# Kernel tuning notes

Hardware: AMD Instinct MI355X
Metric: run time of the kernel (lower is better)

## Reference

```python
import jax, jax.numpy as jnp
import numpy as np

I, H1, H2, O = 64, 1024, 1024, 64

def lstm_cell(x, h, c, W_ih, W_hh, b_ih, b_hh):
    # PyTorch LSTMCell: gates ordered i, f, g, o
    gates = x @ W_ih.T + b_ih + h @ W_hh.T + b_hh  # [B, 4H]
    i, f, g, o = jnp.split(gates, 4, axis=-1)
    i = jax.nn.sigmoid(i)
    f = jax.nn.sigmoid(f)
    g = jnp.tanh(g)
    o = jax.nn.sigmoid(o)
    c_new = f * c + i * g
    h_new = o * jnp.tanh(c_new)
    return h_new, c_new

def setup_inputs() -> dict:
    key = jax.random.key(0)
    ks = jax.random.split(key, 11)
    s1 = 1.0 / np.sqrt(H1)
    s2 = 1.0 / np.sqrt(H2)
    u = lambda k, shape, s: jax.random.uniform(k, shape, jnp.float32, -s, s)
    return {
        "inputs": jax.random.normal(ks[0], (128, 512, I), jnp.float32),
        "W_ih1": u(ks[1], (4 * H1, I), s1),
        "W_hh1": u(ks[2], (4 * H1, H1), s1),
        "b_ih1": u(ks[3], (4 * H1,), s1),
        "b_hh1": u(ks[4], (4 * H1,), s1),
        "W_ih2": u(ks[5], (4 * H2, H1), s2),
        "W_hh2": u(ks[6], (4 * H2, H2), s2),
        "b_ih2": u(ks[7], (4 * H2,), s2),
        "b_hh2": u(ks[8], (4 * H2,), s2),
        "W_out": u(ks[9], (O, H2), s2),
        "b_out": u(ks[10], (O,), s2),
    }

def reference(inputs, W_ih1, W_hh1, b_ih1, b_hh1, W_ih2, W_hh2, b_ih2, b_hh2, W_out, b_out):
    B = inputs.shape[0]
    h1 = jnp.zeros((B, H1), inputs.dtype)
    c1 = jnp.zeros((B, H1), inputs.dtype)
    h2 = jnp.zeros((B, H2), inputs.dtype)
    c2 = jnp.zeros((B, H2), inputs.dtype)

    def step(carry, x_t):
        h1, c1, h2, c2 = carry
        h1, c1 = lstm_cell(x_t, h1, c1, W_ih1, W_hh1, b_ih1, b_hh1)
        h2, c2 = lstm_cell(h1, h2, c2, W_ih2, W_hh2, b_ih2, b_hh2)
        y = h2 @ W_out.T + b_out  # [B, O]
        return (h1, c1, h2, c2), y

    xs = jnp.swapaxes(inputs, 0, 1)  # [T, B, I]
    _, ys = jax.lax.scan(step, (h1, c1, h2, c2), xs)
    return jnp.swapaxes(ys, 0, 1)  # [B, T, O]
```

## Files before the change

### kernel.cpp

```cpp
#include <hip/hip_runtime.h>
#include <hip/hip_fp16.h>

typedef _Float16 half8 __attribute__((ext_vector_type(8)));
typedef float    float4_ __attribute__((ext_vector_type(4)));

#define TSTEPS 512
#define NA 64
#define NB 128
#define NC 8
#define FSTRIDE 32

#define FLA_OFF   0
#define FLB_OFF   8192
#define FLC_OFF   24576
#define H1_OFF    32768
#define H1_PHASE  262144
#define H2_OFF    (H1_OFF + 2 * H1_PHASE)
#define X_OFF     (H2_OFF + 2 * H1_PHASE)
#define X_TSTRIDE 16384
#define ZERO_BYTES X_OFF

__device__ __forceinline__ float fastrcp(float x) {
    float r; asm("v_rcp_f32 %0, %1" : "=v"(r) : "v"(x)); return r;
}
__device__ __forceinline__ float sigf(float x)  { return fastrcp(1.0f + __expf(-x)); }
__device__ __forceinline__ float tanh_(float x) { return 1.0f - 2.0f * fastrcp(1.0f + __expf(2.0f * x)); }

__device__ __forceinline__ half8 wfrag_load(const float* Wa, int lda,
                                            const float* Wb, int ldb,
                                            int split, int row, int k0) {
    const float* s = (k0 < split) ? (Wa + (size_t)row * lda + k0)
                                  : (Wb + (size_t)row * ldb + (k0 - split));
    float4_ lo = *(const float4_*)s;
    float4_ hi = *(const float4_*)(s + 4);
    half8 r;
    r[0] = (_Float16)lo[0]; r[1] = (_Float16)lo[1];
    r[2] = (_Float16)lo[2]; r[3] = (_Float16)lo[3];
    r[4] = (_Float16)hi[0]; r[5] = (_Float16)hi[1];
    r[6] = (_Float16)hi[2]; r[7] = (_Float16)hi[3];
    return r;
}


__device__ __forceinline__ half8 ldg_sc1_16(const void* p) {
    half8 r;
    asm volatile("global_load_dwordx4 %0, %1, off sc1" : "=v"(r) : "v"(p));
    return r;
}

#define VMWAIT8(A) asm volatile("s_waitcnt vmcnt(0)" : \
    "+v"((A)[0]), "+v"((A)[1]), "+v"((A)[2]), "+v"((A)[3]), \
    "+v"((A)[4]), "+v"((A)[5]), "+v"((A)[6]), "+v"((A)[7]) :: "memory")

#define VMWAIT2_N(G, NS) asm volatile("s_waitcnt vmcnt(" NS ")" : \
    "+v"((G)[0]), "+v"((G)[1]) :: "memory")

__device__ __forceinline__ void stg_coh_16(void* p, float4_ v) {
    asm volatile("global_store_dwordx4 %0, %1, off sc0 sc1" :: "v"(p), "v"(v) : "memory");
}

__device__ __forceinline__ void stg_coh_int(void* p, int v) {
    asm volatile("global_store_dword %0, %1, off sc0 sc1" :: "v"(p), "v"(v) : "memory");
}

__device__ __forceinline__ void publish(int* fbase, int idx, int v) {
    asm volatile("s_waitcnt vmcnt(0)" ::: "memory");
    __syncthreads();
    if (threadIdx.x == 0) stg_coh_int(fbase + idx * FSTRIDE, v);
}

__device__ __forceinline__ int ld_flag(const int* f, int idx) {
    return __hip_atomic_load(f + idx * FSTRIDE, __ATOMIC_RELAXED,
                             __HIP_MEMORY_SCOPE_AGENT);
}

__device__ __forceinline__ void waitA(const int* fA, const int* fB, int t) {
    if (threadIdx.x < 64) {
        const int lane = threadIdx.x;
        for (;;) {
            int a  = ld_flag(fA, lane);
            int b0 = ld_flag(fB, lane);
            int b1 = ld_flag(fB, 64 + lane);
            if (__all((a >= t) && (b0 >= t - 1) && (b1 >= t - 1))) break;
            __builtin_amdgcn_s_sleep(1);
        }
    }
    __syncthreads();
}

__device__ __forceinline__ void waitB(const int* fA, const int* fB, const int* fC, int t) {
    if (threadIdx.x < 64) {
        const int lane = threadIdx.x;
        for (;;) {
            int a  = ld_flag(fA, lane);
            int b0 = ld_flag(fB, lane);
            int b1 = ld_flag(fB, 64 + lane);
            int c  = ld_flag(fC, lane & 7);
            if (__all((a >= t + 1) && (b0 >= t) && (b1 >= t) && (c >= t - 1))) break;
            __builtin_amdgcn_s_sleep(1);
        }
    }
    __syncthreads();
}

__device__ __forceinline__ void waitC(const int* fB, int t) {
    if (threadIdx.x < 64) {
        const int lane = threadIdx.x;
        for (;;) {
            int b0 = ld_flag(fB, lane);
            int b1 = ld_flag(fB, 64 + lane);
            if (__all((b0 >= t + 1) && (b1 >= t + 1))) break;
            __builtin_amdgcn_s_sleep(1);
        }
    }
    __syncthreads();
}

__device__ __forceinline__ int swz(int u) {
    return u ^ (((u >> 3) ^ (u >> 7)) & 7);
}

extern "C" __global__ void prep_x(const float* __restrict__ in, char* __restrict__ ws) {
    const int t = blockIdx.x;
    char* X = ws + X_OFF + (size_t)t * X_TSTRIDE;
    for (int idx = threadIdx.x; idx < 8192; idx += 256) {
        int kt = idx >> 12, rem = idx & 4095;
        int quad = rem >> 10, rem2 = rem & 1023;
        int b = rem2 >> 3, j = rem2 & 7;
        int i = kt * 32 + quad * 8 + j;
        float v = in[(size_t)b * 32768 + (size_t)t * 64 + i];
        *(_Float16*)(X + (size_t)idx * 2) = (_Float16)v;
    }
}

extern "C" __global__ __launch_bounds__(256, 1)
void lstm_persistent(const float* __restrict__ Wih1, const float* __restrict__ Whh1,
                     const float* __restrict__ bih1, const float* __restrict__ bhh1,
                     const float* __restrict__ Wih2, const float* __restrict__ Whh2,
                     const float* __restrict__ bih2, const float* __restrict__ bhh2,
                     const float* __restrict__ Wout, const float* __restrict__ bout,
                     char* __restrict__ ws, float* __restrict__ out) {
    const int tid = threadIdx.x;
    const int w = tid >> 6, lane = tid & 63;
    const int quad = lane >> 4, cl = lane & 15;
    const int laneoff = quad * 2048 + cl * 16;
    int* fA = (int*)(ws + FLA_OFF);
    int* fB = (int*)(ws + FLB_OFF);
    int* fC = (int*)(ws + FLC_OFF);
    char* H1 = ws + H1_OFF;
    char* H2 = ws + H2_OFF;
    char* X  = ws + X_OFF;
    const int blk = blockIdx.x;
    __shared__ __align__(16) char smem[143360];

    if (blk < NA) {
        char* wlds = smem;
        unsigned short* stga = (unsigned short*)(smem + 139264);
        const int c0 = blk * 16;
        for (int f = tid; f < 8704; f += 256) {
            int kk = f >> 8, rem = f & 255, nt = rem >> 6, ln = rem & 63;
            int row = nt * 1024 + c0 + (ln & 15);
            int k0 = kk * 32 + (ln >> 4) * 8;
            *(half8*)(wlds + (size_t)f * 16) = wfrag_load(Wih1, 64, Whh1, 1024, 64, row, k0);
        }
        __syncthreads();
        float ba[4];
#pragma unroll
        for (int g = 0; g < 4; ++g) ba[g] = bih1[g * 1024 + c0 + cl] + bhh1[g * 1024 + c0 + cl];
        float cst[2][4];
#pragma unroll
        for (int mi = 0; mi < 2; ++mi)
#pragma unroll
            for (int r = 0; r < 4; ++r) cst[mi][r] = 0.0f;
        const int mtb0 = (2 * w) * 256, mtb1 = (2 * w + 1) * 256;

        for (int t = 0; t < TSTEPS; ++t) {
            waitA(fA, fB, t);

            const char* xb  = X + (size_t)t * X_TSTRIDE;
            const char* h1r = H1 + (((t & 1) ^ 1) ? H1_PHASE : 0);
            char*       h1w = H1 + ((t & 1) ? H1_PHASE : 0);

            half8 af[10][2];
#pragma unroll
            for (int p = 0; p < 10; ++p) {
                const char* bp = (p < 2) ? (xb + p * 8192) : (h1r + (p - 2) * 8192);
                af[p][0] = ldg_sc1_16(bp + laneoff + mtb0);
                af[p][1] = ldg_sc1_16(bp + laneoff + mtb1);
            }
            float4_ acc[2][4];
#pragma unroll
            for (int mi = 0; mi < 2; ++mi)
#pragma unroll
                for (int nt = 0; nt < 4; ++nt) acc[mi][nt] = (float4_){0.f, 0.f, 0.f, 0.f};
#pragma unroll
            for (int kk = 0; kk < 34; ++kk) {
                const int cur = kk % 10;
                if (kk <= 24)      { VMWAIT2_N(af[cur], "18"); }
                else if (kk == 25) { VMWAIT2_N(af[cur], "16"); }
                else if (kk == 26) { VMWAIT2_N(af[cur], "14"); }
                else if (kk == 27) { VMWAIT2_N(af[cur], "12"); }
                else if (kk == 28) { VMWAIT2_N(af[cur], "10"); }
                else if (kk == 29) { VMWAIT2_N(af[cur], "8");  }
                else if (kk == 30) { VMWAIT2_N(af[cur], "6");  }
                else if (kk == 31) { VMWAIT2_N(af[cur], "4");  }
                else if (kk == 32) { VMWAIT2_N(af[cur], "2");  }
                else               { VMWAIT2_N(af[cur], "0");  }
                half8 wl0 = *(const half8*)(wlds + (size_t)((kk * 4 + 0) * 64 + lane) * 16);
                half8 wl1 = *(const half8*)(wlds + (size_t)((kk * 4 + 1) * 64 + lane) * 16);
                half8 wl2 = *(const half8*)(wlds + (size_t)((kk * 4 + 2) * 64 + lane) * 16);
                half8 wl3 = *(const half8*)(wlds + (size_t)((kk * 4 + 3) * 64 + lane) * 16);
                acc[0][0] = __builtin_amdgcn_mfma_f32_16x16x32_f16(af[cur][0], wl0, acc[0][0], 0, 0, 0);
                acc[0][1] = __builtin_amdgcn_mfma_f32_16x16x32_f16(af[cur][0], wl1, acc[0][1], 0, 0, 0);
                acc[0][2] = __builtin_amdgcn_mfma_f32_16x16x32_f16(af[cur][0], wl2, acc[0][2], 0, 0, 0);
                acc[0][3] = __builtin_amdgcn_mfma_f32_16x16x32_f16(af[cur][0], wl3, acc[0][3], 0, 0, 0);
                acc[1][0] = __builtin_amdgcn_mfma_f32_16x16x32_f16(af[cur][1], wl0, acc[1][0], 0, 0, 0);
                acc[1][1] = __builtin_amdgcn_mfma_f32_16x16x32_f16(af[cur][1], wl1, acc[1][1], 0, 0, 0);
                acc[1][2] = __builtin_amdgcn_mfma_f32_16x16x32_f16(af[cur][1], wl2, acc[1][2], 0, 0, 0);
                acc[1][3] = __builtin_amdgcn_mfma_f32_16x16x32_f16(af[cur][1], wl3, acc[1][3], 0, 0, 0);
                if (kk + 10 < 34) {
                    const int kn = kk + 10;
                    const char* bn = (kn < 2) ? (xb + kn * 8192) : (h1r + (kn - 2) * 8192);
                    af[cur][0] = ldg_sc1_16(bn + laneoff + mtb0);
                    af[cur][1] = ldg_sc1_16(bn + laneoff + mtb1);
                }
            }
#pragma unroll
            for (int mi = 0; mi < 2; ++mi) {
#pragma unroll
                for (int r = 0; r < 4; ++r) {
                    float iv = acc[mi][0][r] + ba[0];
                    float fv = acc[mi][1][r] + ba[1];
                    float gv = acc[mi][2][r] + ba[2];
                    float ov = acc[mi][3][r] + ba[3];
                    float c = sigf(fv) * cst[mi][r] + sigf(iv) * tanh_(gv);
                    float h = sigf(ov) * tanh_(c);
                    cst[mi][r] = c;
                    int m = (2 * w + mi) * 16 + quad * 4 + r;
                    int u = ((cl >> 3) << 7) + m;
                    union { _Float16 hh; unsigned short us; } uu;
                    uu.hh = (_Float16)h;
                    stga[swz(u) * 8 + (cl & 7)] = uu.us;
                }
            }
            __syncthreads();
            {
                const int g = tid >> 7, b = tid & 127;
                int u = (g << 7) + b;
                float4_ v = *(const float4_*)(stga + swz(u) * 8);
                char* dst = h1w + ((c0 >> 5) << 13) + ((((c0 >> 3) + g) & 3) << 11) + (b << 4);
                stg_coh_16(dst, v);
            }
            publish(fA, blk, t + 1);
        }
    } else if (blk < NA + NB) {
        char* wldsB = smem;
        unsigned short* stgb = (unsigned short*)(smem + 131072);
        const int bb = blk - NA;
        const int c0 = bb * 8;
        for (int f = tid; f < 8192; f += 256) {
            int kk = f >> 7, rem = f & 127, pr = rem >> 6, ln = rem & 63;
            int cl_ = ln & 15;
            int colB_ = c0 + (cl_ & 7);
            int row = (pr == 0) ? ((cl_ < 8) ? colB_ : (1024 + colB_))
                                : ((cl_ < 8) ? (2048 + colB_) : (3072 + colB_));
            int k0 = kk * 32 + (ln >> 4) * 8;
            *(half8*)(wldsB + (size_t)f * 16) = wfrag_load(Wih2, 1024, Whh2, 1024, 1024, row, k0);
        }
        __syncthreads();
        const int colB = c0 + (cl & 7);
        const float bi = bih2[colB] + bhh2[colB];
        const float bf = bih2[1024 + colB] + bhh2[1024 + colB];
        const float bg = bih2[2048 + colB] + bhh2[2048 + colB];
        const float bo = bih2[3072 + colB] + bhh2[3072 + colB];
        float cst[2][4];
#pragma unroll
        for (int mi = 0; mi < 2; ++mi)
#pragma unroll
            for (int r = 0; r < 4; ++r) cst[mi][r] = 0.0f;
        const bool lolane = (cl & 8) == 0;
        const int mtb0 = (2 * w) * 256, mtb1 = (2 * w + 1) * 256;

        for (int t = 0; t < TSTEPS; ++t) {
            waitB(fA, fB, fC, t);

            const char* h1c = H1 + ((t & 1) ? H1_PHASE : 0);
            const char* h2r = H2 + (((t & 1) ^ 1) ? H1_PHASE : 0);
            char*       h2w = H2 + ((t & 1) ? H1_PHASE : 0);

            half8 af[12][2];
#pragma unroll
            for (int p = 0; p < 12; ++p) {
                const char* bp = h1c + p * 8192;
                af[p][0] = ldg_sc1_16(bp + laneoff + mtb0);
                af[p][1] = ldg_sc1_16(bp + laneoff + mtb1);
            }
            float4_ acc[2][2];
#pragma unroll
            for (int mi = 0; mi < 2; ++mi) {
                acc[mi][0] = (float4_){0.f, 0.f, 0.f, 0.f};
                acc[mi][1] = (float4_){0.f, 0.f, 0.f, 0.f};
            }
#pragma unroll
            for (int kk = 0; kk < 64; ++kk) {
                const int cur = kk % 12;
                if (kk <= 52)      { VMWAIT2_N(af[cur], "22"); }
                else if (kk == 53) { VMWAIT2_N(af[cur], "20"); }
                else if (kk == 54) { VMWAIT2_N(af[cur], "18"); }
                else if (kk == 55) { VMWAIT2_N(af[cur], "16"); }
                else if (kk == 56) { VMWAIT2_N(af[cur], "14"); }
                else if (kk == 57) { VMWAIT2_N(af[cur], "12"); }
                else if (kk == 58) { VMWAIT2_N(af[cur], "10"); }
                else if (kk == 59) { VMWAIT2_N(af[cur], "8");  }
                else if (kk == 60) { VMWAIT2_N(af[cur], "6");  }
                else if (kk == 61) { VMWAIT2_N(af[cur], "4");  }
                else if (kk == 62) { VMWAIT2_N(af[cur], "2");  }
                else               { VMWAIT2_N(af[cur], "0");  }
                half8 wl0 = *(const half8*)(wldsB + (size_t)((kk * 2 + 0) * 64 + lane) * 16);
                half8 wl1 = *(const half8*)(wldsB + (size_t)((kk * 2 + 1) * 64 + lane) * 16);
                acc[0][0] = __builtin_amdgcn_mfma_f32_16x16x32_f16(af[cur][0], wl0, acc[0][0], 0, 0, 0);
                acc[0][1] = __builtin_amdgcn_mfma_f32_16x16x32_f16(af[cur][0], wl1, acc[0][1], 0, 0, 0);
                acc[1][0] = __builtin_amdgcn_mfma_f32_16x16x32_f16(af[cur][1], wl0, acc[1][0], 0, 0, 0);
                acc[1][1] = __builtin_amdgcn_mfma_f32_16x16x32_f16(af[cur][1], wl1, acc[1][1], 0, 0, 0);
                if (kk + 12 < 64) {
                    const int kn = kk + 12;
                    const char* bn = (kn < 32) ? (h1c + kn * 8192) : (h2r + (kn - 32) * 8192);
                    af[cur][0] = ldg_sc1_16(bn + laneoff + mtb0);
                    af[cur][1] = ldg_sc1_16(bn + laneoff + mtb1);
                }
            }
#pragma unroll
            for (int mi = 0; mi < 2; ++mi) {
#pragma unroll
                for (int r = 0; r < 4; ++r) {
                    float d0 = acc[mi][0][r], d1 = acc[mi][1][r];
                    float s0 = __shfl_xor(d0, 8, 64);
                    float s1 = __shfl_xor(d1, 8, 64);
                    float iv = (lolane ? d0 : s0) + bi;
                    float fv = (lolane ? s0 : d0) + bf;
                    float gv = (lolane ? d1 : s1) + bg;
                    float ov = (lolane ? s1 : d1) + bo;
                    float c = sigf(fv) * cst[mi][r] + sigf(iv) * tanh_(gv);
                    float h = sigf(ov) * tanh_(c);
                    cst[mi][r] = c;
                    if (lolane) {
                        int m = (2 * w + mi) * 16 + quad * 4 + r;
                        union { _Float16 hh; unsigned short us; } uu;
                        uu.hh = (_Float16)h;
                        stgb[swz(m) * 8 + (cl & 7)] = uu.us;
                    }
                }
            }
            __syncthreads();
            if (tid < 128) {
                const int b = tid;
                float4_ v = *(const float4_*)(stgb + swz(b) * 8);
                char* dst = h2w + ((c0 >> 5) << 13) + (((c0 >> 3) & 3) << 11) + (b << 4);
                stg_coh_16(dst, v);
            }
            publish(fB, bb, t + 1);
        }
    } else {
        float* redc = (float*)smem;
        const int cb = blk - NA - NB;
        const int kbase = w * 8;
        half8 wfr[4][8];
#pragma unroll
        for (int nt = 0; nt < 4; ++nt) {
            int row = nt * 16 + cl;
#pragma unroll
            for (int kk = 0; kk < 8; ++kk)
                wfr[nt][kk] = wfrag_load(Wout, 1024, Wout, 1024, 1 << 30, row, (kbase + kk) * 32 + quad * 8);
        }
        const float bo_ = bout[w * 16 + cl];

        for (int t = 0; t < TSTEPS; ++t) {
            waitC(fB, t);
            const char* h2c = H2 + ((t & 1) ? H1_PHASE : 0);
            float4_ acc[4];
#pragma unroll
            for (int nt = 0; nt < 4; ++nt) acc[nt] = (float4_){0.f, 0.f, 0.f, 0.f};
            half8 af[8];
#pragma unroll
            for (int kk = 0; kk < 8; ++kk)
                af[kk] = ldg_sc1_16(h2c + (kbase + kk) * 8192 + laneoff + cb * 256);
            VMWAIT8(af);
#pragma unroll
            for (int kk = 0; kk < 8; ++kk)
#pragma unroll
                for (int nt = 0; nt < 4; ++nt)
                    acc[nt] = __builtin_amdgcn_mfma_f32_16x16x32_f16(af[kk], wfr[nt][kk], acc[nt], 0, 0, 0);
#pragma unroll
            for (int r = 0; r < 4; ++r) {
                if (w != r) *(float4_*)&redc[(w * 64 + lane) * 4] = acc[r];
                __syncthreads();
                if (w == r) {
#pragma unroll
                    for (int wo = 0; wo < 4; ++wo) if (wo != r)
                        acc[r] += *(const float4_*)&redc[(wo * 64 + lane) * 4];
                }
                __syncthreads();
            }
            float4_ myy = acc[0];
#pragma unroll
            for (int r = 1; r < 4; ++r) if (w == r) myy = acc[r];
#pragma unroll
            for (int r = 0; r < 4; ++r) {
                int m = cb * 16 + quad * 4 + r;
                out[(size_t)m * 32768 + (size_t)t * 64 + (w * 16 + cl)] = myy[r] + bo_;
            }
            publish(fC, cb, t + 1);
        }
    }
}

extern "C" void kernel_launch(void* const* d_in, const int* in_sizes, int n_in,
                              void* d_out, int out_size, void* d_ws, size_t ws_size,
                              hipStream_t stream) {
    const float* inp  = (const float*)d_in[0];
    const float* Wih1 = (const float*)d_in[1];
    const float* Whh1 = (const float*)d_in[2];
    const float* bih1 = (const float*)d_in[3];
    const float* bhh1 = (const float*)d_in[4];
    const float* Wih2 = (const float*)d_in[5];
    const float* Whh2 = (const float*)d_in[6];
    const float* bih2 = (const float*)d_in[7];
    const float* bhh2 = (const float*)d_in[8];
    const float* Wout = (const float*)d_in[9];
    const float* bout = (const float*)d_in[10];
    char* ws = (char*)d_ws;

    hipMemsetAsync(d_ws, 0, ZERO_BYTES, stream);
    prep_x<<<TSTEPS, 256, 0, stream>>>(inp, ws);
    lstm_persistent<<<NA + NB + NC, 256, 0, stream>>>(Wih1, Whh1, bih1, bhh1,
                                                      Wih2, Whh2, bih2, bhh2,
                                                      Wout, bout, ws, (float*)d_out);
}
```

Measured before the change: 4.270 ms.

## Split layer-2 wait so recurrent h2 matmul overlaps waiting on layer-1 output

Layer 2 used to wait for both its own recurrent dependencies and the fresh layer-1 h1 before starting any work. The wait is now split in two. It first waits only on the h2/flag dependencies and computes the W_hh2·h2 half of the gates. Only then does it wait for layer-1 h1 and compute the W_ih2·h1 half, which takes layer-1 latency off the critical path. Prefetch depth also grows (14 buffers in layer 1, 16 in layer 2), which raises register pressure and could reduce occupancy or cause spills.

```diff
diff --git a/kernel.cpp b/kernel.cpp
--- a/kernel.cpp
+++ b/kernel.cpp
@@ -88,15 +88,26 @@
     __syncthreads();
 }
 
-__device__ __forceinline__ void waitB(const int* fA, const int* fB, const int* fC, int t) {
+__device__ __forceinline__ void waitB1(const int* fB, const int* fC, int t) {
     if (threadIdx.x < 64) {
         const int lane = threadIdx.x;
         for (;;) {
-            int a  = ld_flag(fA, lane);
             int b0 = ld_flag(fB, lane);
             int b1 = ld_flag(fB, 64 + lane);
             int c  = ld_flag(fC, lane & 7);
-            if (__all((a >= t + 1) && (b0 >= t) && (b1 >= t) && (c >= t - 1))) break;
+            if (__all((b0 >= t) && (b1 >= t) && (c >= t - 1))) break;
+            __builtin_amdgcn_s_sleep(1);
+        }
+    }
+    __syncthreads();
+}
+
+__device__ __forceinline__ void waitB2(const int* fA, int t) {
+    if (threadIdx.x < 64) {
+        const int lane = threadIdx.x;
+        for (;;) {
+            int a = ld_flag(fA, lane);
+            if (__all(a >= t + 1)) break;
             __builtin_amdgcn_s_sleep(1);
         }
     }
@@ -181,9 +192,9 @@
             const char* h1r = H1 + (((t & 1) ^ 1) ? H1_PHASE : 0);
             char*       h1w = H1 + ((t & 1) ? H1_PHASE : 0);
 
-            half8 af[10][2];
-#pragma unroll
-            for (int p = 0; p < 10; ++p) {
+            half8 af[14][2];
+#pragma unroll
+            for (int p = 0; p < 14; ++p) {
                 const char* bp = (p < 2) ? (xb + p * 8192) : (h1r + (p - 2) * 8192);
                 af[p][0] = ldg_sc1_16(bp + laneoff + mtb0);
                 af[p][1] = ldg_sc1_16(bp + laneoff + mtb1);
@@ -195,8 +206,12 @@
                 for (int nt = 0; nt < 4; ++nt) acc[mi][nt] = (float4_){0.f, 0.f, 0.f, 0.f};
 #pragma unroll
             for (int kk = 0; kk < 34; ++kk) {
-                const int cur = kk % 10;
-                if (kk <= 24)      { VMWAIT2_N(af[cur], "18"); }
+                const int cur = kk % 14;
+                if (kk <= 20)      { VMWAIT2_N(af[cur], "26"); }
+                else if (kk == 21) { VMWAIT2_N(af[cur], "24"); }
+                else if (kk == 22) { VMWAIT2_N(af[cur], "22"); }
+                else if (kk == 23) { VMWAIT2_N(af[cur], "20"); }
+                else if (kk == 24) { VMWAIT2_N(af[cur], "18"); }
                 else if (kk == 25) { VMWAIT2_N(af[cur], "16"); }
                 else if (kk == 26) { VMWAIT2_N(af[cur], "14"); }
                 else if (kk == 27) { VMWAIT2_N(af[cur], "12"); }
@@ -218,9 +233,9 @@
                 acc[1][1] = __builtin_amdgcn_mfma_f32_16x16x32_f16(af[cur][1], wl1, acc[1][1], 0, 0, 0);
                 acc[1][2] = __builtin_amdgcn_mfma_f32_16x16x32_f16(af[cur][1], wl2, acc[1][2], 0, 0, 0);
                 acc[1][3] = __builtin_amdgcn_mfma_f32_16x16x32_f16(af[cur][1], wl3, acc[1][3], 0, 0, 0);
-                if (kk + 10 < 34) {
-                    const int kn = kk + 10;
-                    const char* bn = (kn < 2) ? (xb + kn * 8192) : (h1r + (kn - 2) * 8192);
+                if (kk + 14 < 34) {
+                    const int kn = kk + 14;
+                    const char* bn = h1r + (kn - 2) * 8192;
                     af[cur][0] = ldg_sc1_16(bn + laneoff + mtb0);
                     af[cur][1] = ldg_sc1_16(bn + laneoff + mtb1);
                 }
@@ -282,53 +297,98 @@
         const int mtb0 = (2 * w) * 256, mtb1 = (2 * w + 1) * 256;
 
         for (int t = 0; t < TSTEPS; ++t) {
-            waitB(fA, fB, fC, t);
-
             const char* h1c = H1 + ((t & 1) ? H1_PHASE : 0);
             const char* h2r = H2 + (((t & 1) ^ 1) ? H1_PHASE : 0);
             char*       h2w = H2 + ((t & 1) ? H1_PHASE : 0);
 
-            half8 af[12][2];
-#pragma unroll
-            for (int p = 0; p < 12; ++p) {
-                const char* bp = h1c + p * 8192;
-                af[p][0] = ldg_sc1_16(bp + laneoff + mtb0);
-                af[p][1] = ldg_sc1_16(bp + laneoff + mtb1);
-            }
             float4_ acc[2][2];
 #pragma unroll
             for (int mi = 0; mi < 2; ++mi) {
                 acc[mi][0] = (float4_){0.f, 0.f, 0.f, 0.f};
                 acc[mi][1] = (float4_){0.f, 0.f, 0.f, 0.f};
             }
-#pragma unroll
-            for (int kk = 0; kk < 64; ++kk) {
-                const int cur = kk % 12;
-                if (kk <= 52)      { VMWAIT2_N(af[cur], "22"); }
-                else if (kk == 53) { VMWAIT2_N(af[cur], "20"); }
-                else if (kk == 54) { VMWAIT2_N(af[cur], "18"); }
-                else if (kk == 55) { VMWAIT2_N(af[cur], "16"); }
-                else if (kk == 56) { VMWAIT2_N(af[cur], "14"); }
-                else if (kk == 57) { VMWAIT2_N(af[cur], "12"); }
-                else if (kk == 58) { VMWAIT2_N(af[cur], "10"); }
-                else if (kk == 59) { VMWAIT2_N(af[cur], "8");  }
-                else if (kk == 60) { VMWAIT2_N(af[cur], "6");  }
-                else if (kk == 61) { VMWAIT2_N(af[cur], "4");  }
-                else if (kk == 62) { VMWAIT2_N(af[cur], "2");  }
-                else               { VMWAIT2_N(af[cur], "0");  }
+            half8 af[16][2];
+
+            waitB1(fB, fC, t);
+#pragma unroll
+            for (int p = 0; p < 16; ++p) {
+                const char* bp = h2r + p * 8192;
+                af[p][0] = ldg_sc1_16(bp + laneoff + mtb0);
+                af[p][1] = ldg_sc1_16(bp + laneoff + mtb1);
+            }
+#pragma unroll
+            for (int i = 0; i < 32; ++i) {
+                const int kk = 32 + i;
+                const int cur = i & 15;
+                if (i <= 16)      { VMWAIT2_N(af[cur], "30"); }
+                else if (i == 17) { VMWAIT2_N(af[cur], "28"); }
+                else if (i == 18) { VMWAIT2_N(af[cur], "26"); }
+                else if (i == 19) { VMWAIT2_N(af[cur], "24"); }
+                else if (i == 20) { VMWAIT2_N(af[cur], "22"); }
+                else if (i == 21) { VMWAIT2_N(af[cur], "20"); }
+                else if (i == 22) { VMWAIT2_N(af[cur], "18"); }
+                else if (i == 23) { VMWAIT2_N(af[cur], "16"); }
+                else if (i == 24) { VMWAIT2_N(af[cur], "14"); }
+                else if (i == 25) { VMWAIT2_N(af[cur], "12"); }
+                else if (i == 26) { VMWAIT2_N(af[cur], "10"); }
+                else if (i == 27) { VMWAIT2_N(af[cur], "8");  }
+                else if (i == 28) { VMWAIT2_N(af[cur], "6");  }
+                else if (i == 29) { VMWAIT2_N(af[cur], "4");  }
+                else if (i == 30) { VMWAIT2_N(af[cur], "2");  }
+                else              { VMWAIT2_N(af[cur], "0");  }
                 half8 wl0 = *(const half8*)(wldsB + (size_t)((kk * 2 + 0) * 64 + lane) * 16);
                 half8 wl1 = *(const half8*)(wldsB + (size_t)((kk * 2 + 1) * 64 + lane) * 16);
                 acc[0][0] = __builtin_amdgcn_mfma_f32_16x16x32_f16(af[cur][0], wl0, acc[0][0], 0, 0, 0);
                 acc[0][1] = __builtin_amdgcn_mfma_f32_16x16x32_f16(af[cur][0], wl1, acc[0][1], 0, 0, 0);
                 acc[1][0] = __builtin_amdgcn_mfma_f32_16x16x32_f16(af[cur][1], wl0, acc[1][0], 0, 0, 0);
                 acc[1][1] = __builtin_amdgcn_mfma_f32_16x16x32_f16(af[cur][1], wl1, acc[1][1], 0, 0, 0);
-                if (kk + 12 < 64) {
-                    const int kn = kk + 12;
-                    const char* bn = (kn < 32) ? (h1c + kn * 8192) : (h2r + (kn - 32) * 8192);
+                if (i + 16 < 32) {
+                    const char* bn = h2r + (i + 16) * 8192;
                     af[cur][0] = ldg_sc1_16(bn + laneoff + mtb0);
                     af[cur][1] = ldg_sc1_16(bn + laneoff + mtb1);
                 }
             }
+
+            waitB2(fA, t);
+#pragma unroll
+            for (int p = 0; p < 16; ++p) {
+                const char* bp = h1c + p * 8192;
+                af[p][0] = ldg_sc1_16(bp + laneoff + mtb0);
+                af[p][1] = ldg_sc1_16(bp + laneoff + mtb1);
+            }
+#pragma unroll
+            for (int i = 0; i < 32; ++i) {
+                const int kk = i;
+                const int cur = i & 15;
+                if (i <= 16)      { VMWAIT2_N(af[cur], "30"); }
+                else if (i == 17) { VMWAIT2_N(af[cur], "28"); }
+                else if (i == 18) { VMWAIT2_N(af[cur], "26"); }
+                else if (i == 19) { VMWAIT2_N(af[cur], "24"); }
+                else if (i == 20) { VMWAIT2_N(af[cur], "22"); }
+                else if (i == 21) { VMWAIT2_N(af[cur], "20"); }
+                else if (i == 22) { VMWAIT2_N(af[cur], "18"); }
+                else if (i == 23) { VMWAIT2_N(af[cur], "16"); }
+                else if (i == 24) { VMWAIT2_N(af[cur], "14"); }
+                else if (i == 25) { VMWAIT2_N(af[cur], "12"); }
+                else if (i == 26) { VMWAIT2_N(af[cur], "10"); }
+                else if (i == 27) { VMWAIT2_N(af[cur], "8");  }
+                else if (i == 28) { VMWAIT2_N(af[cur], "6");  }
+                else if (i == 29) { VMWAIT2_N(af[cur], "4");  }
+                else if (i == 30) { VMWAIT2_N(af[cur], "2");  }
+                else              { VMWAIT2_N(af[cur], "0");  }
+                half8 wl0 = *(const half8*)(wldsB + (size_t)((kk * 2 + 0) * 64 + lane) * 16);
+                half8 wl1 = *(const half8*)(wldsB + (size_t)((kk * 2 + 1) * 64 + lane) * 16);
+                acc[0][0] = __builtin_amdgcn_mfma_f32_16x16x32_f16(af[cur][0], wl0, acc[0][0], 0, 0, 0);
+                acc[0][1] = __builtin_amdgcn_mfma_f32_16x16x32_f16(af[cur][0], wl1, acc[0][1], 0, 0, 0);
+                acc[1][0] = __builtin_amdgcn_mfma_f32_16x16x32_f16(af[cur][1], wl0, acc[1][0], 0, 0, 0);
+                acc[1][1] = __builtin_amdgcn_mfma_f32_16x16x32_f16(af[cur][1], wl1, acc[1][1], 0, 0, 0);
+                if (i + 16 < 32) {
+                    const char* bn = h1c + (i + 16) * 8192;
+                    af[cur][0] = ldg_sc1_16(bn + laneoff + mtb0);
+                    af[cur][1] = ldg_sc1_16(bn + laneoff + mtb1);
+                }
+            }
+
 #pragma unroll
             for (int mi = 0; mi < 2; ++mi) {
 #pragma unroll
```

After: 4.448 ms. +4.2%, slower.
